# Optimization experiments

Hardware: AMD Instinct MI355X
Metric: run time of the kernel (lower is better)

The kernel has to match this reference:

```python
import jax, jax.numpy as jnp
import numpy as np

DIM = 1024
HEADS = 16
HEAD_DIM = 64
ROT_DIM = HEAD_DIM // 2  # RotaryEmbedding(dim=head_dim//2): rotates first 32 dims only
B, T, H, W = 2, 32, 18, 32


def setup_inputs() -> dict:
    key = jax.random.key(0)
    k1, k2, k3 = jax.random.split(key, 3)
    x = jax.random.normal(k1, (B, T, H, W, DIM), dtype=jnp.float32)
    w_qkv = jax.random.normal(k2, (3 * HEADS * HEAD_DIM, DIM), dtype=jnp.float32) * 0.02
    w_out = jax.random.normal(k3, (DIM, HEADS * HEAD_DIM), dtype=jnp.float32) * 0.02
    b_out = jnp.zeros((DIM,), dtype=jnp.float32)
    return {"x": x, "w_qkv": w_qkv, "w_out": w_out, "b_out": b_out}


def _rope(t, pos):
    # t: [N, h, T, d]. lucidrains convention: interleaved pairs, rotate first ROT_DIM dims.
    freqs = 1.0 / (10000.0 ** (jnp.arange(0, ROT_DIM, 2, dtype=jnp.float32) / ROT_DIM))  # [ROT_DIM/2]
    ang = pos[:, None] * freqs[None, :]          # [T, ROT_DIM/2]
    ang = jnp.repeat(ang, 2, axis=-1)            # [T, ROT_DIM] (each freq repeated for its pair)
    cos, sin = jnp.cos(ang), jnp.sin(ang)
    x_rot, x_pass = t[..., :ROT_DIM], t[..., ROT_DIM:]
    xr = x_rot.reshape(x_rot.shape[:-1] + (ROT_DIM // 2, 2))
    rot = jnp.stack([-xr[..., 1], xr[..., 0]], axis=-1).reshape(x_rot.shape)  # rotate_half
    return jnp.concatenate([x_rot * cos + rot * sin, x_pass], axis=-1)


def reference(x, w_qkv, w_out, b_out):
    b, t, h, w, d = x.shape
    # fused QKV projection (bias=False)
    qkv = jnp.einsum('bthwd,ed->bthwe', x, w_qkv)
    q, k, v = jnp.split(qkv, 3, axis=-1)

    def to_heads(u):
        # 'B T H W (h d) -> (B H W) h T d'
        u = u.reshape(b, t, h, w, HEADS, HEAD_DIM)
        return u.transpose(0, 2, 3, 4, 1, 5).reshape(b * h * w, HEADS, t, HEAD_DIM)

    q, k, v = to_heads(q), to_heads(k), to_heads(v)
    pos = jnp.arange(t, dtype=jnp.float32)
    q = _rope(q, pos)
    k = _rope(k, pos)

    scale = HEAD_DIM ** -0.5
    scores = jnp.einsum('nhqd,nhkd->nhqk', q, k) * scale  # [BHW, h, T, T]
    causal = jnp.tril(jnp.ones((t, t), dtype=bool))
    scores = jnp.where(causal, scores, -jnp.inf)
    attn = jax.nn.softmax(scores, axis=-1)
    o = jnp.einsum('nhqk,nhkd->nhqd', attn, v)
    # '(B H W) h T d -> B T H W (h d)'
    o = o.reshape(b, h, w, HEADS, t, HEAD_DIM).transpose(0, 4, 1, 2, 3, 5)
    o = o.reshape(b, t, h, w, HEADS * HEAD_DIM)
    return o @ w_out.T + b_out
```

## Files before the change

### kernel.cpp

```cpp
#include <hip/hip_runtime.h>
#include <cstdint>
#include <cstddef>

typedef __bf16 bf16;
typedef __attribute__((ext_vector_type(8))) bf16  bf16x8;
typedef __attribute__((ext_vector_type(4))) bf16  bf16x4;
typedef __attribute__((ext_vector_type(4))) float f32x4;

#define B_SZ   2
#define T_SZ   32
#define H_SZ   18
#define W_SZ   32
#define DIM    1024
#define NHEAD  16
#define HDIM   64
#define E3     3072
#define M_TOT  36864
#define T_STRIDE 576

__global__ void taa_cvt_bf16(const float* __restrict__ s, bf16* __restrict__ d, int n4) {
    int i = blockIdx.x * 256 + threadIdx.x;
    if (i >= n4) return;
    float4 v = ((const float4*)s)[i];
    bf16x4 o;
    o.x = (bf16)v.x; o.y = (bf16)v.y; o.z = (bf16)v.z; o.w = (bf16)v.w;
    ((bf16x4*)d)[i] = o;
}

__device__ __forceinline__ void async_copy_16(const bf16* g, bf16* l) {
    __builtin_amdgcn_global_load_lds((__attribute__((address_space(1))) void*)g,
                                     (__attribute__((address_space(3))) void*)l,
                                     16, 0, 0);
}

template<bool OUT_BF16>
__global__ __launch_bounds__(256)
void taa_gemm_bt(const bf16* __restrict__ A, const bf16* __restrict__ B,
                 void* __restrict__ Cout, const float* __restrict__ bias,
                 int N, int K) {
    __shared__ __align__(16) bf16 sA[128 * 32];
    __shared__ __align__(16) bf16 sB[128 * 32];

    const int tid  = threadIdx.x;
    const int bm   = blockIdx.y * 128;
    const int bn   = blockIdx.x * 128;
    const int lane = tid & 63;
    const int wv   = tid >> 6;
    const int wm   = (wv >> 1) * 64;
    const int wn   = (wv & 1) * 64;
    const int fr   = lane & 15;
    const int fq   = lane >> 4;
    const int kswz = (fr >> 1) & 3;

    f32x4 acc[4][4];
#pragma unroll
    for (int i = 0; i < 4; i++)
#pragma unroll
        for (int j = 0; j < 4; j++) acc[i][j] = (f32x4){0.f, 0.f, 0.f, 0.f};

    const int srow   = tid >> 2;
    const int schunk = (tid & 3) ^ ((srow >> 1) & 3);
    const bf16* gA = A + (size_t)(bm + srow) * K + schunk * 8;
    const bf16* gB = B + (size_t)(bn + srow) * K + schunk * 8;
    bf16* lA = &sA[tid * 8];
    bf16* lB = &sB[tid * 8];
    const size_t rowskip = (size_t)64 * K;

    for (int kt = 0; kt < K; kt += 32) {
        __syncthreads();
        async_copy_16(gA,            lA);
        async_copy_16(gA + rowskip,  lA + 2048);
        async_copy_16(gB,            lB);
        async_copy_16(gB + rowskip,  lB + 2048);
        gA += 32; gB += 32;
        __syncthreads();

        bf16x8 af[4], bfr[4];
#pragma unroll
        for (int i = 0; i < 4; i++)
            af[i] = *(const bf16x8*)&sA[(wm + i * 16 + fr) * 32 + (fq ^ kswz) * 8];
#pragma unroll
        for (int j = 0; j < 4; j++)
            bfr[j] = *(const bf16x8*)&sB[(wn + j * 16 + fr) * 32 + (fq ^ kswz) * 8];
#pragma unroll
        for (int i = 0; i < 4; i++)
#pragma unroll
            for (int j = 0; j < 4; j++)
                acc[i][j] = __builtin_amdgcn_mfma_f32_16x16x32_bf16(af[i], bfr[j], acc[i][j], 0, 0, 0);
    }

    if constexpr (OUT_BF16) {
        bf16* C = (bf16*)Cout;
#pragma unroll
        for (int i = 0; i < 4; i++)
#pragma unroll
            for (int j = 0; j < 4; j++)
#pragma unroll
                for (int r = 0; r < 4; r++) {
                    int row = bm + wm + i * 16 + fq * 4 + r;
                    int col = bn + wn + j * 16 + fr;
                    C[(size_t)row * N + col] = (bf16)acc[i][j][r];
                }
    } else {
        float* C = (float*)Cout;
#pragma unroll
        for (int i = 0; i < 4; i++)
#pragma unroll
            for (int j = 0; j < 4; j++)
#pragma unroll
                for (int r = 0; r < 4; r++) {
                    int row = bm + wm + i * 16 + fq * 4 + r;
                    int col = bn + wn + j * 16 + fr;
                    C[(size_t)row * N + col] = acc[i][j][r] + bias[col];
                }
    }
}

__global__ __launch_bounds__(64)
void taa_attn_mfma(const bf16* __restrict__ qkv, bf16* __restrict__ o) {
    __shared__ __align__(16) bf16 sQ[32 * 72];
    __shared__ __align__(16) bf16 sK[32 * 72];
    __shared__ __align__(16) bf16 sVt[64 * 40];
    __shared__ __align__(16) bf16 sP[32 * 40];

    const int lane = threadIdx.x;
    const int bid  = blockIdx.x;
    const int head = bid & 15;
    const int n    = bid >> 4;
    const int w_sp = n & 31;
    const int h_sp = (n >> 5) % 18;
    const int b    = n / (18 * 32);
    const int m0   = b * 18432 + h_sp * 32 + w_sp;

    {
        const int tl = lane >> 3;
        const int dl = (lane & 7) * 8;
#pragma unroll
        for (int it = 0; it < 4; ++it) {
            const int t = it * 8 + tl;
            const size_t rb = (size_t)(m0 + t * T_STRIDE) * E3 + head * 64 + dl;
            bf16x8 q8 = *(const bf16x8*)(qkv + rb);
            bf16x8 k8 = *(const bf16x8*)(qkv + rb + 1024);
            bf16x8 v8 = *(const bf16x8*)(qkv + rb + 2048);
            float qf[8], kf[8];
#pragma unroll
            for (int j = 0; j < 8; j++) { qf[j] = (float)q8[j]; kf[j] = (float)k8[j]; }
            if (dl < 32) {
#pragma unroll
                for (int p = 0; p < 4; p++) {
                    const int fi = dl / 2 + p;
                    float freq = exp2f(-(float)fi * 0.830482024f);
                    float ang  = (float)t * freq;
                    float s, c;
                    sincosf(ang, &s, &c);
                    float a = qf[2 * p], bb = qf[2 * p + 1];
                    qf[2 * p]     = a * c - bb * s;
                    qf[2 * p + 1] = bb * c + a * s;
                    a = kf[2 * p]; bb = kf[2 * p + 1];
                    kf[2 * p]     = a * c - bb * s;
                    kf[2 * p + 1] = bb * c + a * s;
                }
            }
            bf16x8 qo, ko;
#pragma unroll
            for (int j = 0; j < 8; j++) { qo[j] = (bf16)qf[j]; ko[j] = (bf16)kf[j]; }
            *(bf16x8*)&sQ[t * 72 + dl] = qo;
            *(bf16x8*)&sK[t * 72 + dl] = ko;
#pragma unroll
            for (int j = 0; j < 8; j++) sVt[(dl + j) * 40 + t] = v8[j];
        }
    }
    __syncthreads();

    const int fr = lane & 15;
    const int fq = lane >> 4;

    f32x4 S[2][2];
#pragma unroll
    for (int mt = 0; mt < 2; mt++)
#pragma unroll
        for (int nt = 0; nt < 2; nt++) S[mt][nt] = (f32x4){0.f, 0.f, 0.f, 0.f};

    bf16x8 kb0[2], kb1[2];
#pragma unroll
    for (int nt = 0; nt < 2; nt++) {
        kb0[nt] = *(const bf16x8*)&sK[(nt * 16 + fr) * 72 + fq * 8];
        kb1[nt] = *(const bf16x8*)&sK[(nt * 16 + fr) * 72 + 32 + fq * 8];
    }
#pragma unroll
    for (int mt = 0; mt < 2; mt++) {
        bf16x8 a0 = *(const bf16x8*)&sQ[(mt * 16 + fr) * 72 + fq * 8];
        bf16x8 a1 = *(const bf16x8*)&sQ[(mt * 16 + fr) * 72 + 32 + fq * 8];
#pragma unroll
        for (int nt = 0; nt < 2; nt++) {
            S[mt][nt] = __builtin_amdgcn_mfma_f32_16x16x32_bf16(a0, kb0[nt], S[mt][nt], 0, 0, 0);
            S[mt][nt] = __builtin_amdgcn_mfma_f32_16x16x32_bf16(a1, kb1[nt], S[mt][nt], 0, 0, 0);
        }
    }

    float P[2][2][4];
#pragma unroll
    for (int mt = 0; mt < 2; mt++) {
#pragma unroll
        for (int r = 0; r < 4; r++) {
            const int row = mt * 16 + fq * 4 + r;
            float s0 = S[mt][0][r] * 0.125f;
            float s1 = S[mt][1][r] * 0.125f;
            if (fr > row)      s0 = -1e30f;
            if (16 + fr > row) s1 = -1e30f;
            float mx = fmaxf(s0, s1);
#pragma unroll
            for (int mk = 1; mk <= 8; mk <<= 1) mx = fmaxf(mx, __shfl_xor(mx, mk, 64));
            float e0 = __expf(s0 - mx);
            float e1 = __expf(s1 - mx);
            float sm = e0 + e1;
#pragma unroll
            for (int mk = 1; mk <= 8; mk <<= 1) sm += __shfl_xor(sm, mk, 64);
            float inv = 1.0f / sm;
            P[mt][0][r] = e0 * inv;
            P[mt][1][r] = e1 * inv;
        }
    }

#pragma unroll
    for (int mt = 0; mt < 2; mt++)
#pragma unroll
        for (int nt = 0; nt < 2; nt++)
#pragma unroll
            for (int r = 0; r < 4; r++)
                sP[(mt * 16 + fq * 4 + r) * 40 + nt * 16 + fr] = (bf16)P[mt][nt][r];
    __syncthreads();

    f32x4 O[2][4];
#pragma unroll
    for (int mt = 0; mt < 2; mt++)
#pragma unroll
        for (int dt = 0; dt < 4; dt++) O[mt][dt] = (f32x4){0.f, 0.f, 0.f, 0.f};
#pragma unroll
    for (int mt = 0; mt < 2; mt++) {
        bf16x8 a = *(const bf16x8*)&sP[(mt * 16 + fr) * 40 + fq * 8];
#pragma unroll
        for (int dt = 0; dt < 4; dt++) {
            bf16x8 bv = *(const bf16x8*)&sVt[(dt * 16 + fr) * 40 + fq * 8];
            O[mt][dt] = __builtin_amdgcn_mfma_f32_16x16x32_bf16(a, bv, O[mt][dt], 0, 0, 0);
        }
    }

#pragma unroll
    for (int mt = 0; mt < 2; mt++)
#pragma unroll
        for (int dt = 0; dt < 4; dt++)
#pragma unroll
            for (int r = 0; r < 4; r++) {
                const int t = mt * 16 + fq * 4 + r;
                const int d = dt * 16 + fr;
                o[(size_t)(m0 + t * T_STRIDE) * DIM + head * 64 + d] = (bf16)O[mt][dt][r];
            }
}

extern "C" void kernel_launch(void* const* d_in, const int* in_sizes, int n_in,
                              void* d_out, int out_size, void* d_ws, size_t ws_size,
                              hipStream_t stream) {
    const float* x     = (const float*)d_in[0];
    const float* w_qkv = (const float*)d_in[1];
    const float* w_out = (const float*)d_in[2];
    const float* b_out = (const float*)d_in[3];

    char* ws = (char*)d_ws;
    bf16* x_b    = (bf16*)(ws + 0);
    bf16* wqkv_b = (bf16*)(ws + 75497472);
    bf16* wout_b = (bf16*)(ws + 81788928);
    bf16* qkv_b  = (bf16*)(ws + 83886080);
    bf16* o_b    = (bf16*)(ws + 310378496);

    taa_cvt_bf16<<<(M_TOT * DIM / 4 + 255) / 256, 256, 0, stream>>>(x, x_b, M_TOT * DIM / 4);
    taa_cvt_bf16<<<(E3 * DIM / 4 + 255) / 256, 256, 0, stream>>>(w_qkv, wqkv_b, E3 * DIM / 4);
    taa_cvt_bf16<<<(DIM * DIM / 4 + 255) / 256, 256, 0, stream>>>(w_out, wout_b, DIM * DIM / 4);

    taa_gemm_bt<true><<<dim3(E3 / 128, M_TOT / 128), 256, 0, stream>>>(
        x_b, wqkv_b, (void*)qkv_b, nullptr, E3, DIM);

    taa_attn_mfma<<<1152 * 16, 64, 0, stream>>>(qkv_b, o_b);

    taa_gemm_bt<false><<<dim3(DIM / 128, M_TOT / 128), 256, 0, stream>>>(
        o_b, wout_b, d_out, b_out, DIM, DIM);
}
```

Baseline: 757.4 us.

## Replace GEMM with 256x256 double-buffered pipelined MFMA kernel with grid swizzle

Replaces the 128x128 single-buffered GEMM with a 256x256 tile, 512-thread kernel that double-buffers K=64 slices in LDS. Global-to-LDS async loads for the tile after next are interleaved between four MFMA quadrant phases, using explicit barriers, waitcnts and setprio. It also adds an XOR LDS swizzle and an XCD-aware block-index swizzle. The aim is to hide global latency and raise MFMA utilisation in both projections, at the cost of heavy hand scheduling and a larger register and LDS footprint.

```diff
diff --git a/kernel.cpp b/kernel.cpp
--- a/kernel.cpp
+++ b/kernel.cpp
@@ -17,6 +17,8 @@
 #define E3     3072
 #define M_TOT  36864
 #define T_STRIDE 576
+#define GK     1024
+#define NKT    16
 
 __global__ void taa_cvt_bf16(const float* __restrict__ s, bf16* __restrict__ d, int n4) {
     int i = blockIdx.x * 256 + threadIdx.x;
@@ -33,86 +35,204 @@
                                      16, 0, 0);
 }
 
+#define MFMA16(a, b, c) __builtin_amdgcn_mfma_f32_16x16x32_bf16((a), (b), (c), 0, 0, 0)
+
 template<bool OUT_BF16>
-__global__ __launch_bounds__(256)
-void taa_gemm_bt(const bf16* __restrict__ A, const bf16* __restrict__ B,
-                 void* __restrict__ Cout, const float* __restrict__ bias,
-                 int N, int K) {
-    __shared__ __align__(16) bf16 sA[128 * 32];
-    __shared__ __align__(16) bf16 sB[128 * 32];
+__global__ __launch_bounds__(512, 2)
+void taa_gemm256(const bf16* __restrict__ A, const bf16* __restrict__ Bm,
+                 void* __restrict__ Cout, const float* __restrict__ bias, int N) {
+    __shared__ __align__(16) bf16 sA[2][2][8192];
+    __shared__ __align__(16) bf16 sB[2][2][8192];
 
     const int tid  = threadIdx.x;
-    const int bm   = blockIdx.y * 128;
-    const int bn   = blockIdx.x * 128;
     const int lane = tid & 63;
     const int wv   = tid >> 6;
-    const int wm   = (wv >> 1) * 64;
-    const int wn   = (wv & 1) * 64;
+    const int wm   = wv >> 2;
+    const int wn   = wv & 3;
     const int fr   = lane & 15;
     const int fq   = lane >> 4;
-    const int kswz = (fr >> 1) & 3;
-
-    f32x4 acc[4][4];
-#pragma unroll
-    for (int i = 0; i < 4; i++)
-#pragma unroll
-        for (int j = 0; j < 4; j++) acc[i][j] = (f32x4){0.f, 0.f, 0.f, 0.f};
-
-    const int srow   = tid >> 2;
-    const int schunk = (tid & 3) ^ ((srow >> 1) & 3);
-    const bf16* gA = A + (size_t)(bm + srow) * K + schunk * 8;
-    const bf16* gB = B + (size_t)(bn + srow) * K + schunk * 8;
-    bf16* lA = &sA[tid * 8];
-    bf16* lB = &sB[tid * 8];
-    const size_t rowskip = (size_t)64 * K;
-
-    for (int kt = 0; kt < K; kt += 32) {
-        __syncthreads();
-        async_copy_16(gA,            lA);
-        async_copy_16(gA + rowskip,  lA + 2048);
-        async_copy_16(gB,            lB);
-        async_copy_16(gB + rowskip,  lB + 2048);
-        gA += 32; gB += 32;
-        __syncthreads();
-
-        bf16x8 af[4], bfr[4];
+
+    const int ntn = N >> 8;
+    const int nwg = gridDim.x;
+    const int bid = blockIdx.x;
+    const int swz = (bid & 7) * (nwg >> 3) + (bid >> 3);
+    const int bm  = (swz / ntn) << 8;
+    const int bn  = (swz % ntn) << 8;
+
+    const int srow = tid >> 3;
+    const int scol = ((tid & 7) ^ (srow & 7)) << 3;
+    const bf16* gA0 = A  + (size_t)(bm + srow) * GK + scol;
+    const bf16* gB0 = Bm + (size_t)(bn + srow) * GK + scol;
+
+    const int swx = (fr & 7) << 4;
+    const int cs0 = (fq * 16) ^ swx;
+    const int cs1 = (64 + fq * 16) ^ swx;
+
+    f32x4 acc[2][2][4][2];
+#pragma unroll
+    for (int ms = 0; ms < 2; ms++)
+#pragma unroll
+        for (int ns = 0; ns < 2; ns++)
+#pragma unroll
+            for (int i = 0; i < 4; i++)
+#pragma unroll
+                for (int j = 0; j < 2; j++)
+                    acc[ms][ns][i][j] = (f32x4){0.f, 0.f, 0.f, 0.f};
+
+    auto stage = [&](const bf16* g0, bf16* lbase, int h, int kt) {
+        const bf16* g = g0 + (size_t)(h * 128) * GK + kt * 64;
+        async_copy_16(g,                    lbase + h * 8192 + tid * 8);
+        async_copy_16(g + (size_t)64 * GK,  lbase + h * 8192 + 4096 + tid * 8);
+    };
+
+    stage(gB0, &sB[0][0][0], 0, 0); stage(gB0, &sB[0][0][0], 1, 0);
+    stage(gA0, &sA[0][0][0], 0, 0); stage(gA0, &sA[0][0][0], 1, 0);
+    stage(gB0, &sB[1][0][0], 0, 1); stage(gB0, &sB[1][0][0], 1, 1);
+    stage(gA0, &sA[1][0][0], 0, 1); stage(gA0, &sA[1][0][0], 1, 1);
+    asm volatile("s_waitcnt vmcnt(8)" ::: "memory");
+    __builtin_amdgcn_s_barrier();
+    asm volatile("" ::: "memory");
+
+    bf16x8 af[4][2];
+    bf16x8 bfr[2][2][2];
+
+#pragma unroll 2
+    for (int kt = 0; kt < NKT; ++kt) {
+        const int buf = kt & 1;
+        const char* ab = (const char*)&sA[buf][wm][0] + fr * 128;
+        const char* bb = (const char*)&sB[buf][wn >> 1][0] + ((wn & 1) * 64 + fr) * 128;
+        const bool st = (kt + 2 < NKT);
+
+#pragma unroll
+        for (int i = 0; i < 4; i++) {
+            af[i][0] = *(const bf16x8*)(ab + i * 2048 + cs0);
+            af[i][1] = *(const bf16x8*)(ab + i * 2048 + cs1);
+        }
+#pragma unroll
+        for (int j = 0; j < 2; j++) {
+            bfr[0][j][0] = *(const bf16x8*)(bb + j * 2048 + cs0);
+            bfr[0][j][1] = *(const bf16x8*)(bb + j * 2048 + cs1);
+        }
+        asm volatile("" ::: "memory");
+        __builtin_amdgcn_s_barrier();
+        asm volatile("s_waitcnt lgkmcnt(0)" ::: "memory");
+        __builtin_amdgcn_sched_barrier(0);
+        __builtin_amdgcn_s_setprio(1);
 #pragma unroll
         for (int i = 0; i < 4; i++)
-            af[i] = *(const bf16x8*)&sA[(wm + i * 16 + fr) * 32 + (fq ^ kswz) * 8];
-#pragma unroll
-        for (int j = 0; j < 4; j++)
-            bfr[j] = *(const bf16x8*)&sB[(wn + j * 16 + fr) * 32 + (fq ^ kswz) * 8];
+#pragma unroll
+            for (int j = 0; j < 2; j++) {
+                acc[0][0][i][j] = MFMA16(af[i][0], bfr[0][j][0], acc[0][0][i][j]);
+                acc[0][0][i][j] = MFMA16(af[i][1], bfr[0][j][1], acc[0][0][i][j]);
+            }
+        __builtin_amdgcn_s_setprio(0);
+        asm volatile("" ::: "memory");
+        __builtin_amdgcn_s_barrier();
+        asm volatile("" ::: "memory");
+
+#pragma unroll
+        for (int j = 0; j < 2; j++) {
+            bfr[1][j][0] = *(const bf16x8*)(bb + 4096 + j * 2048 + cs0);
+            bfr[1][j][1] = *(const bf16x8*)(bb + 4096 + j * 2048 + cs1);
+        }
+        asm volatile("" ::: "memory");
+        __builtin_amdgcn_s_barrier();
+        asm volatile("s_waitcnt lgkmcnt(0)" ::: "memory");
+        __builtin_amdgcn_sched_barrier(0);
+        __builtin_amdgcn_s_setprio(1);
 #pragma unroll
         for (int i = 0; i < 4; i++)
 #pragma unroll
-            for (int j = 0; j < 4; j++)
-                acc[i][j] = __builtin_amdgcn_mfma_f32_16x16x32_bf16(af[i], bfr[j], acc[i][j], 0, 0, 0);
+            for (int j = 0; j < 2; j++) {
+                acc[0][1][i][j] = MFMA16(af[i][0], bfr[1][j][0], acc[0][1][i][j]);
+                acc[0][1][i][j] = MFMA16(af[i][1], bfr[1][j][1], acc[0][1][i][j]);
+            }
+        __builtin_amdgcn_s_setprio(0);
+        asm volatile("" ::: "memory");
+        __builtin_amdgcn_s_barrier();
+        asm volatile("" ::: "memory");
+
+#pragma unroll
+        for (int i = 0; i < 4; i++) {
+            af[i][0] = *(const bf16x8*)(ab + 8192 + i * 2048 + cs0);
+            af[i][1] = *(const bf16x8*)(ab + 8192 + i * 2048 + cs1);
+        }
+        if (st) {
+            stage(gB0, &sB[buf][0][0], 0, kt + 2);
+            stage(gB0, &sB[buf][0][0], 1, kt + 2);
+        }
+        asm volatile("" ::: "memory");
+        __builtin_amdgcn_s_barrier();
+        asm volatile("s_waitcnt lgkmcnt(0)" ::: "memory");
+        __builtin_amdgcn_sched_barrier(0);
+        __builtin_amdgcn_s_setprio(1);
+#pragma unroll
+        for (int i = 0; i < 4; i++)
+#pragma unroll
+            for (int j = 0; j < 2; j++) {
+                acc[1][1][i][j] = MFMA16(af[i][0], bfr[1][j][0], acc[1][1][i][j]);
+                acc[1][1][i][j] = MFMA16(af[i][1], bfr[1][j][1], acc[1][1][i][j]);
+            }
+        __builtin_amdgcn_s_setprio(0);
+        asm volatile("" ::: "memory");
+        __builtin_amdgcn_s_barrier();
+        asm volatile("" ::: "memory");
+
+        if (st) {
+            stage(gA0, &sA[buf][0][0], 0, kt + 2);
+            stage(gA0, &sA[buf][0][0], 1, kt + 2);
+        }
+        asm volatile("" ::: "memory");
+        __builtin_amdgcn_s_barrier();
+        __builtin_amdgcn_sched_barrier(0);
+        __builtin_amdgcn_s_setprio(1);
+#pragma unroll
+        for (int i = 0; i < 4; i++)
+#pragma unroll
+            for (int j = 0; j < 2; j++) {
+                acc[1][0][i][j] = MFMA16(af[i][0], bfr[0][j][0], acc[1][0][i][j]);
+                acc[1][0][i][j] = MFMA16(af[i][1], bfr[0][j][1], acc[1][0][i][j]);
+            }
+        __builtin_amdgcn_s_setprio(0);
+        if (kt < NKT - 2) asm volatile("s_waitcnt vmcnt(8)" ::: "memory");
+        else              asm volatile("s_waitcnt vmcnt(0)" ::: "memory");
+        asm volatile("" ::: "memory");
+        __builtin_amdgcn_s_barrier();
+        asm volatile("" ::: "memory");
     }
 
     if constexpr (OUT_BF16) {
         bf16* C = (bf16*)Cout;
 #pragma unroll
-        for (int i = 0; i < 4; i++)
-#pragma unroll
-            for (int j = 0; j < 4; j++)
-#pragma unroll
-                for (int r = 0; r < 4; r++) {
-                    int row = bm + wm + i * 16 + fq * 4 + r;
-                    int col = bn + wn + j * 16 + fr;
-                    C[(size_t)row * N + col] = (bf16)acc[i][j][r];
-                }
+        for (int ms = 0; ms < 2; ms++)
+#pragma unroll
+            for (int ns = 0; ns < 2; ns++)
+#pragma unroll
+                for (int i = 0; i < 4; i++)
+#pragma unroll
+                    for (int j = 0; j < 2; j++)
+#pragma unroll
+                        for (int r = 0; r < 4; r++) {
+                            const int row = bm + wm * 128 + ms * 64 + i * 16 + fq * 4 + r;
+                            const int col = bn + wn * 64 + ns * 32 + j * 16 + fr;
+                            C[(size_t)row * N + col] = (bf16)acc[ms][ns][i][j][r];
+                        }
     } else {
         float* C = (float*)Cout;
 #pragma unroll
-        for (int i = 0; i < 4; i++)
-#pragma unroll
-            for (int j = 0; j < 4; j++)
-#pragma unroll
-                for (int r = 0; r < 4; r++) {
-                    int row = bm + wm + i * 16 + fq * 4 + r;
-                    int col = bn + wn + j * 16 + fr;
-                    C[(size_t)row * N + col] = acc[i][j][r] + bias[col];
-                }
+        for (int ms = 0; ms < 2; ms++)
+#pragma unroll
+            for (int ns = 0; ns < 2; ns++)
+#pragma unroll
+                for (int i = 0; i < 4; i++)
+#pragma unroll
+                    for (int j = 0; j < 2; j++)
+#pragma unroll
+                        for (int r = 0; r < 4; r++) {
+                            const int row = bm + wm * 128 + ms * 64 + i * 16 + fq * 4 + r;
+                            const int col = bn + wn * 64 + ns * 32 + j * 16 + fr;
+                            C[(size_t)row * N + col] = acc[ms][ns][i][j][r] + bias[col];
+                        }
     }
 }
 
@@ -277,11 +397,11 @@
     taa_cvt_bf16<<<(E3 * DIM / 4 + 255) / 256, 256, 0, stream>>>(w_qkv, wqkv_b, E3 * DIM / 4);
     taa_cvt_bf16<<<(DIM * DIM / 4 + 255) / 256, 256, 0, stream>>>(w_out, wout_b, DIM * DIM / 4);
 
-    taa_gemm_bt<true><<<dim3(E3 / 128, M_TOT / 128), 256, 0, stream>>>(
-        x_b, wqkv_b, (void*)qkv_b, nullptr, E3, DIM);
+    taa_gemm256<true><<<dim3((M_TOT / 256) * (E3 / 256)), 512, 0, stream>>>(
+        x_b, wqkv_b, (void*)qkv_b, nullptr, E3);
 
     taa_attn_mfma<<<1152 * 16, 64, 0, stream>>>(qkv_b, o_b);
 
-    taa_gemm_bt<false><<<dim3(DIM / 128, M_TOT / 128), 256, 0, stream>>>(
-        o_b, wout_b, d_out, b_out, DIM, DIM);
+    taa_gemm256<false><<<dim3((M_TOT / 256) * (DIM / 256)), 512, 0, stream>>>(
+        o_b, wout_b, d_out, b_out, DIM);
 }
```

Measured after the change: 719.2 us. 5.0% less time.
